# Kernel optimization log

Hardware: AMD Instinct MI355X
Metric: run time of the kernel (lower is better)

The kernel has to match this reference:

```python
import jax, jax.numpy as jnp
import numpy as np

B, S, D, H = 8, 577, 768, 12
P, KW = 576, 32            # num_patches, num_wormholes
HD = D // H                # head_dim = 64
SCALE = HD ** -0.5
TEMP = 0.1
GRID = 24                  # sqrt(P)
CANTOR_W = 0.3


def _cantor_position_bias():
    idx = np.arange(P)
    xg, yg = idx % GRID, idx // GRID
    s = xg + yg
    z = (s * (s + 1) // 2 + yg).astype(np.float32)
    fp = z / max(z.max(), 1.0)
    aff = 1.0 - np.abs(fp[None, :] - fp[:, None])
    np.fill_diagonal(aff, -1e9)
    return jnp.asarray(aff * CANTOR_W, dtype=jnp.float32)


def setup_inputs() -> dict:
    key = jax.random.key(0)
    ks = jax.random.split(key, 12)
    MLP = 4 * D
    w = lambda k, sh: jax.random.normal(k, sh, dtype=jnp.float32) * 0.02
    return {
        "x": jax.random.normal(ks[0], (B, S, D), dtype=jnp.float32),
        "g1": jnp.ones((D,), jnp.float32), "b1": jnp.zeros((D,), jnp.float32),
        "wq": w(ks[1], (D, D)), "bq": jnp.zeros((D,), jnp.float32),
        "wk": w(ks[2], (D, D)), "bk": jnp.zeros((D,), jnp.float32),
        "pos_bias": _cantor_position_bias(),
        "w_qkv": w(ks[3], (D, 3 * D)), "b_qkv": jnp.zeros((3 * D,), jnp.float32),
        "w_proj": w(ks[4], (D, D)), "b_proj": jnp.zeros((D,), jnp.float32),
        "g2": jnp.ones((D,), jnp.float32), "b2": jnp.zeros((D,), jnp.float32),
        "w_mlp1": w(ks[5], (D, 4 * D)), "b_mlp1": jnp.zeros((4 * D,), jnp.float32),
        "w_mlp2": w(ks[6], (4 * D, D)), "b_mlp2": jnp.zeros((D,), jnp.float32),
    }


def _ln(x, g, b):
    m = x.mean(-1, keepdims=True)
    v = x.var(-1, keepdims=True)
    return (x - m) / jnp.sqrt(v + 1e-5) * g + b


def _l2norm(x):  # F.normalize(dim=-1)
    return x / jnp.maximum(jnp.linalg.norm(x, axis=-1, keepdims=True), 1e-12)


def reference(x, g1, b1, wq, bq, wk, bk, pos_bias, w_qkv, b_qkv,
              w_proj, b_proj, g2, b2, w_mlp1, b_mlp1, w_mlp2, b_mlp2):
    xn = _ln(x, g1, b1)

    # --- learned wormhole router (content top-k) ---
    xp = xn[:, 1:, :]                                     # [B,P,D]
    q = _l2norm(xp @ wq + bq)
    k = _l2norm(xp @ wk + bk)
    scores = jnp.einsum('bpd,bqd->bpq', q, k) + pos_bias  # [B,P,P]
    scores = jnp.where(jnp.eye(P, dtype=bool), -1e9, scores) / TEMP
    topk_scores, routes = jax.lax.top_k(scores, KW)       # [B,P,K]
    weights = jax.nn.softmax(topk_scores, axis=-1)

    # --- qkv ---
    qkv = (xn @ w_qkv + b_qkv).reshape(B, S, 3, H, HD).transpose(2, 0, 3, 1, 4)
    Q, Kf, V = qkv[0], qkv[1], qkv[2]                     # [B,H,S,HD]

    # --- CLS: dense attention over all tokens ---
    attn_cls = jax.nn.softmax(jnp.einsum('bhqd,bhkd->bhqk', Q[:, :, :1], Kf) * SCALE, -1)
    out_cls = jnp.einsum('bhqk,bhkd->bhqd', attn_cls, V)  # [B,H,1,HD]

    # --- patches: sparse attention over gathered wormhole K/V ---
    Qp, Kp, Vp = Q[:, :, 1:], Kf[:, :, 1:], V[:, :, 1:]   # [B,H,P,HD]
    bi = jnp.arange(B)[:, None, None, None]
    hi = jnp.arange(H)[None, :, None, None]
    ri = routes[:, None, :, :]                            # [B,1,P,K] -> bcast [B,H,P,K]
    Kg = Kp[bi, hi, ri]                                   # [B,H,P,K,HD]
    Vg = Vp[bi, hi, ri]
    sp = jnp.einsum('bhpd,bhpkd->bhpk', Qp, Kg) * SCALE
    sp = sp + jnp.maximum(jnp.log(weights), -10.0)[:, None]
    ap = jax.nn.softmax(sp, axis=-1)
    out_p = jnp.einsum('bhpk,bhpkd->bhpd', ap, Vg)        # [B,H,P,HD]

    out = jnp.concatenate([out_cls, out_p], axis=2)       # [B,H,S,HD]
    out = out.transpose(0, 2, 1, 3).reshape(B, S, D)
    x = x + (out @ w_proj + b_proj)

    # --- MLP ---
    h = jax.nn.gelu(_ln(x, g2, b2) @ w_mlp1 + b_mlp1, approximate=False)
    x = x + (h @ w_mlp2 + b_mlp2)
    return x
```

## Files before the change

kernel.cpp:

```cpp
#include <hip/hip_runtime.h>
#include <math.h>

#define B_  8
#define S_  577
#define D_  768
#define H_  12
#define P_  576
#define KW_ 32
#define HD_ 64
constexpr int   MS       = B_ * S_;
constexpr int   MP       = B_ * P_;
constexpr float SCALE_   = 0.125f;
constexpr float INV_TEMP = 10.0f;

typedef __attribute__((ext_vector_type(8))) short bf16x8;
typedef __attribute__((ext_vector_type(4))) float f32x4;

__device__ __forceinline__ unsigned short f2bf(float f) {
  unsigned int x = __float_as_uint(f);
  x += 0x7fffu + ((x >> 16) & 1u);
  return (unsigned short)(x >> 16);
}
__device__ __forceinline__ float bf2f(unsigned short h) {
  return __uint_as_float((unsigned int)h << 16);
}
__device__ __forceinline__ void gl_lds16(const unsigned short* g,
                                         unsigned short* l) {
  __builtin_amdgcn_global_load_lds(
      (const __attribute__((address_space(1))) void*)g,
      (__attribute__((address_space(3))) void*)l, 16, 0, 0);
}
__device__ __forceinline__ void unpack8(bf16x8 v, float* f) {
  union { bf16x8 v8; unsigned int w[4]; } u;
  u.v8 = v;
#pragma unroll
  for (int i = 0; i < 4; ++i) {
    f[2 * i]     = __uint_as_float(u.w[i] << 16);
    f[2 * i + 1] = __uint_as_float(u.w[i] & 0xffff0000u);
  }
}

template <bool LO>
__global__ __launch_bounds__(256) void ln_rows_bf(
    const float* __restrict__ X, const float* __restrict__ g,
    const float* __restrict__ bta, unsigned short* __restrict__ Yh,
    unsigned short* __restrict__ Yl) {
  const int r = blockIdx.x, tid = threadIdx.x;
  const float* row = X + (long)r * D_;
  float v[3];
  float s = 0.f, sq = 0.f;
#pragma unroll
  for (int t = 0; t < 3; ++t) {
    v[t] = row[tid + t * 256];
    s += v[t];
    sq = fmaf(v[t], v[t], sq);
  }
#pragma unroll
  for (int off = 32; off; off >>= 1) {
    s  += __shfl_xor(s, off);
    sq += __shfl_xor(sq, off);
  }
  __shared__ float rs[4], rq[4];
  if ((tid & 63) == 0) { rs[tid >> 6] = s; rq[tid >> 6] = sq; }
  __syncthreads();
  s  = rs[0] + rs[1] + rs[2] + rs[3];
  sq = rq[0] + rq[1] + rq[2] + rq[3];
  const float m   = s * (1.f / D_);
  const float var = sq * (1.f / D_) - m * m;
  const float inv = rsqrtf(var + 1e-5f);
#pragma unroll
  for (int t = 0; t < 3; ++t) {
    const int c = tid + t * 256;
    const float y = (v[t] - m) * inv * g[c] + bta[c];
    const unsigned short h = f2bf(y);
    Yh[(long)r * D_ + c] = h;
    if (LO) Yl[(long)r * D_ + c] = f2bf(y - bf2f(h));
  }
}

__global__ __launch_bounds__(256) void l2norm_hl(
    const float* __restrict__ X, unsigned short* __restrict__ Yh,
    unsigned short* __restrict__ Yl) {
  const int r = blockIdx.x, tid = threadIdx.x;
  const float* row = X + (long)r * D_;
  float v[3];
  float sq = 0.f;
#pragma unroll
  for (int t = 0; t < 3; ++t) {
    v[t] = row[tid + t * 256];
    sq = fmaf(v[t], v[t], sq);
  }
#pragma unroll
  for (int off = 32; off; off >>= 1) sq += __shfl_xor(sq, off);
  __shared__ float rq[4];
  if ((tid & 63) == 0) rq[tid >> 6] = sq;
  __syncthreads();
  sq = rq[0] + rq[1] + rq[2] + rq[3];
  const float sc = 1.f / fmaxf(sqrtf(sq), 1e-12f);
#pragma unroll
  for (int t = 0; t < 3; ++t) {
    const float y = v[t] * sc;
    const unsigned short h = f2bf(y);
    Yh[(long)r * D_ + tid + t * 256] = h;
    Yl[(long)r * D_ + tid + t * 256] = f2bf(y - bf2f(h));
  }
}

__global__ __launch_bounds__(256) void transpose_hl(
    const float* __restrict__ W, unsigned short* __restrict__ Th,
    unsigned short* __restrict__ Tl, int K, int N, int rowoff) {
  __shared__ float t[32][33];
  const int tx = threadIdx.x & 31, ty = threadIdx.x >> 5;
  const int n0 = blockIdx.x * 32, k0 = blockIdx.y * 32;
#pragma unroll
  for (int i = ty; i < 32; i += 8)
    t[i][tx] = W[(long)(k0 + i) * N + n0 + tx];
  __syncthreads();
#pragma unroll
  for (int i = ty; i < 32; i += 8) {
    const float w = t[tx][i];
    const unsigned short h = f2bf(w);
    const long o = (long)(rowoff + n0 + i) * K + k0 + tx;
    Th[o] = h;
    if (Tl) Tl[o] = f2bf(w - bf2f(h));
  }
}

enum { BEPI_QKV = 0, BEPI_ADD = 1, BEPI_GELU = 2 };

template <int EPI>
__global__ __launch_bounds__(256, 2) void gemm_bf16(
    const unsigned short* __restrict__ A, const unsigned short* __restrict__ Wt,
    const float* __restrict__ bias, const float* __restrict__ R,
    float* __restrict__ C, unsigned short* __restrict__ Cbf,
    int M, int N, int K,
    unsigned short* __restrict__ Qb, unsigned short* __restrict__ Kb,
    unsigned short* __restrict__ Vb) {
  constexpr int BK = 32;
  __shared__ __align__(16) unsigned short ldsA[128 * BK];
  __shared__ __align__(16) unsigned short ldsB[128 * BK];
  const int tid = threadIdx.x, wave = tid >> 6, lane = tid & 63;
  const int wr = wave >> 1, wc = wave & 1;
  const int l16 = lane & 15, l4 = lane >> 4;
  const int bn = blockIdx.x, bm = blockIdx.y;
  const int row0 = bm * 128;

  f32x4 acc[4][4];
#pragma unroll
  for (int i = 0; i < 4; ++i)
#pragma unroll
    for (int j = 0; j < 4; ++j) acc[i][j] = (f32x4){0.f, 0.f, 0.f, 0.f};

  const int c0 = tid, c1 = tid + 256;
  int ar0 = row0 + (c0 >> 2); if (ar0 > M - 1) ar0 = M - 1;
  int ar1 = row0 + (c1 >> 2); if (ar1 > M - 1) ar1 = M - 1;
  const unsigned short* ga0 = A + (long)ar0 * K + ((c0 & 3) << 3);
  const unsigned short* ga1 = A + (long)ar1 * K + ((c1 & 3) << 3);
  const unsigned short* gb0 = Wt + (long)(bn * 128 + (c0 >> 2)) * K + ((c0 & 3) << 3);
  const unsigned short* gb1 = Wt + (long)(bn * 128 + (c1 >> 2)) * K + ((c1 & 3) << 3);

  for (int k0 = 0; k0 < K; k0 += BK) {
    __syncthreads();
    gl_lds16(ga0 + k0, ldsA + c0 * 8);
    gl_lds16(ga1 + k0, ldsA + c1 * 8);
    gl_lds16(gb0 + k0, ldsB + c0 * 8);
    gl_lds16(gb1 + k0, ldsB + c1 * 8);
    __syncthreads();
    bf16x8 af[4], bfr[4];
#pragma unroll
    for (int i = 0; i < 4; ++i)
      af[i] = *(const bf16x8*)(ldsA + (wr * 64 + i * 16 + l16) * BK + l4 * 8);
#pragma unroll
    for (int j = 0; j < 4; ++j)
      bfr[j] = *(const bf16x8*)(ldsB + (wc * 64 + j * 16 + l16) * BK + l4 * 8);
#pragma unroll
    for (int i = 0; i < 4; ++i)
#pragma unroll
      for (int j = 0; j < 4; ++j)
        acc[i][j] = __builtin_amdgcn_mfma_f32_16x16x32_bf16(af[i], bfr[j],
                                                            acc[i][j], 0, 0, 0);
  }

#pragma unroll
  for (int j = 0; j < 4; ++j) {
    const int gcol = bn * 128 + wc * 64 + j * 16 + l16;
    const float bb = bias[gcol];
#pragma unroll
    for (int i = 0; i < 4; ++i) {
      const int grow0 = row0 + wr * 64 + i * 16 + l4 * 4;
#pragma unroll
      for (int r = 0; r < 4; ++r) {
        const int grow = grow0 + r;
        if (grow >= M) continue;
        float v = acc[i][j][r] + bb;
        if (EPI == BEPI_GELU) {
          v = 0.5f * v * (1.f + erff(v * 0.70710678118654752f));
          Cbf[(long)grow * N + gcol] = f2bf(v);
        } else if (EPI == BEPI_ADD) {
          C[(long)grow * N + gcol] = v + R[(long)grow * N + gcol];
        } else {
          const int t   = gcol / (H_ * HD_);
          const int rem = gcol - t * (H_ * HD_);
          const int h   = rem >> 6;
          const int d   = rem & 63;
          const int b   = grow / S_;
          const int ss  = grow - b * S_;
          unsigned short* dst = (t == 0 ? Qb : (t == 1 ? Kb : Vb));
          dst[(((long)(b * H_ + h) * S_ + ss) << 6) + d] = f2bf(v);
        }
      }
    }
  }
}

__global__ __launch_bounds__(256, 2) void gemm_rproj(
    const unsigned short* __restrict__ Ahi, const unsigned short* __restrict__ Alo,
    const unsigned short* __restrict__ Whi, const unsigned short* __restrict__ Wlo,
    const float* __restrict__ bq, const float* __restrict__ bk,
    float* __restrict__ qout, float* __restrict__ kout) {
  constexpr int BK = 32, K = D_;
  __shared__ __align__(16) unsigned short ldsA[128 * BK];
  __shared__ __align__(16) unsigned short ldsB[128 * BK];
  const int tid = threadIdx.x, wave = tid >> 6, lane = tid & 63;
  const int wr = wave >> 1, wc = wave & 1;
  const int l16 = lane & 15, l4 = lane >> 4;
  const int bn = blockIdx.x, bm = blockIdx.y;
  const int row0 = bm * 128;

  f32x4 acc[4][4];
#pragma unroll
  for (int i = 0; i < 4; ++i)
#pragma unroll
    for (int j = 0; j < 4; ++j) acc[i][j] = (f32x4){0.f, 0.f, 0.f, 0.f};

  const int c0 = tid, c1 = tid + 256;
  const int r0 = row0 + (c0 >> 2), r1 = row0 + (c1 >> 2);
  const long aoff0 = (long)(r0 + r0 / P_ + 1) * K + ((c0 & 3) << 3);
  const long aoff1 = (long)(r1 + r1 / P_ + 1) * K + ((c1 & 3) << 3);
  const long boff0 = (long)(bn * 128 + (c0 >> 2)) * K + ((c0 & 3) << 3);
  const long boff1 = (long)(bn * 128 + (c1 >> 2)) * K + ((c1 & 3) << 3);

  for (int ph = 0; ph < 3; ++ph) {
    const unsigned short* As = (ph < 2) ? Ahi : Alo;
    const unsigned short* Bs = (ph == 1) ? Wlo : Whi;
    for (int k0 = 0; k0 < K; k0 += BK) {
      __syncthreads();
      gl_lds16(As + aoff0 + k0, ldsA + c0 * 8);
      gl_lds16(As + aoff1 + k0, ldsA + c1 * 8);
      gl_lds16(Bs + boff0 + k0, ldsB + c0 * 8);
      gl_lds16(Bs + boff1 + k0, ldsB + c1 * 8);
      __syncthreads();
      bf16x8 af[4], bfr[4];
#pragma unroll
      for (int i = 0; i < 4; ++i)
        af[i] = *(const bf16x8*)(ldsA + (wr * 64 + i * 16 + l16) * BK + l4 * 8);
#pragma unroll
      for (int j = 0; j < 4; ++j)
        bfr[j] = *(const bf16x8*)(ldsB + (wc * 64 + j * 16 + l16) * BK + l4 * 8);
#pragma unroll
      for (int i = 0; i < 4; ++i)
#pragma unroll
        for (int j = 0; j < 4; ++j)
          acc[i][j] = __builtin_amdgcn_mfma_f32_16x16x32_bf16(af[i], bfr[j],
                                                              acc[i][j], 0, 0, 0);
    }
  }

#pragma unroll
  for (int j = 0; j < 4; ++j) {
    const int gcol = bn * 128 + wc * 64 + j * 16 + l16;
    const float bb = (gcol < D_) ? bq[gcol] : bk[gcol - D_];
#pragma unroll
    for (int i = 0; i < 4; ++i) {
      const int grow0 = row0 + wr * 64 + i * 16 + l4 * 4;
#pragma unroll
      for (int r = 0; r < 4; ++r) {
        const int grow = grow0 + r;
        const float v = acc[i][j][r] + bb;
        if (gcol < D_) qout[(long)grow * D_ + gcol] = v;
        else           kout[(long)grow * D_ + gcol - D_] = v;
      }
    }
  }
}

__global__ __launch_bounds__(256, 2) void gemm_scores(
    const unsigned short* __restrict__ Qh, const unsigned short* __restrict__ Ql,
    const unsigned short* __restrict__ Kh, const unsigned short* __restrict__ Kl,
    const float* __restrict__ pos, float* __restrict__ sc) {
  constexpr int BK = 32, K = D_;
  __shared__ __align__(16) unsigned short ldsA[128 * BK];
  __shared__ __align__(16) unsigned short ldsB[128 * BK];
  const int tid = threadIdx.x, wave = tid >> 6, lane = tid & 63;
  const int wr = wave >> 1, wc = wave & 1;
  const int l16 = lane & 15, l4 = lane >> 4;
  const int bn = blockIdx.x, bm = blockIdx.y, b = blockIdx.z;
  const long base = (long)b * P_ * K;
  const int row0 = bm * 128;

  f32x4 acc[4][4];
#pragma unroll
  for (int i = 0; i < 4; ++i)
#pragma unroll
    for (int j = 0; j < 4; ++j) acc[i][j] = (f32x4){0.f, 0.f, 0.f, 0.f};

  const int c0 = tid, c1 = tid + 256;
  int r0 = row0 + (c0 >> 2); if (r0 > P_ - 1) r0 = P_ - 1;
  int r1 = row0 + (c1 >> 2); if (r1 > P_ - 1) r1 = P_ - 1;
  int n0 = bn * 128 + (c0 >> 2); if (n0 > P_ - 1) n0 = P_ - 1;
  int n1 = bn * 128 + (c1 >> 2); if (n1 > P_ - 1) n1 = P_ - 1;
  const long aoff0 = base + (long)r0 * K + ((c0 & 3) << 3);
  const long aoff1 = base + (long)r1 * K + ((c1 & 3) << 3);
  const long boff0 = base + (long)n0 * K + ((c0 & 3) << 3);
  const long boff1 = base + (long)n1 * K + ((c1 & 3) << 3);

  for (int ph = 0; ph < 3; ++ph) {
    const unsigned short* As = (ph < 2) ? Qh : Ql;
    const unsigned short* Bs = (ph == 1) ? Kl : Kh;
    for (int k0 = 0; k0 < K; k0 += BK) {
      __syncthreads();
      gl_lds16(As + aoff0 + k0, ldsA + c0 * 8);
      gl_lds16(As + aoff1 + k0, ldsA + c1 * 8);
      gl_lds16(Bs + boff0 + k0, ldsB + c0 * 8);
      gl_lds16(Bs + boff1 + k0, ldsB + c1 * 8);
      __syncthreads();
      bf16x8 af[4], bfr[4];
#pragma unroll
      for (int i = 0; i < 4; ++i)
        af[i] = *(const bf16x8*)(ldsA + (wr * 64 + i * 16 + l16) * BK + l4 * 8);
#pragma unroll
      for (int j = 0; j < 4; ++j)
        bfr[j] = *(const bf16x8*)(ldsB + (wc * 64 + j * 16 + l16) * BK + l4 * 8);
#pragma unroll
      for (int i = 0; i < 4; ++i)
#pragma unroll
        for (int j = 0; j < 4; ++j)
          acc[i][j] = __builtin_amdgcn_mfma_f32_16x16x32_bf16(af[i], bfr[j],
                                                              acc[i][j], 0, 0, 0);
    }
  }

#pragma unroll
  for (int j = 0; j < 4; ++j) {
    const int gj = bn * 128 + wc * 64 + j * 16 + l16;
    if (gj >= P_) continue;
#pragma unroll
    for (int i = 0; i < 4; ++i) {
      const int grow0 = row0 + wr * 64 + i * 16 + l4 * 4;
#pragma unroll
      for (int r = 0; r < 4; ++r) {
        const int gi = grow0 + r;
        if (gi >= P_) continue;
        const float s = (gi == gj) ? -1e9f : acc[i][j][r] + pos[(long)gi * P_ + gj];
        sc[((long)b * P_ + gi) * P_ + gj] = s * INV_TEMP;
      }
    }
  }
}

__global__ __launch_bounds__(64) void topk_route(
    const float* __restrict__ sc, int* __restrict__ routes,
    float* __restrict__ logw) {
  const int row = blockIdx.x, lane = threadIdx.x;
  const float* srow = sc + (long)row * P_;
  float v[9];
#pragma unroll
  for (int t = 0; t < 9; ++t) v[t] = srow[lane + (t << 6)];
  float selv = 0.f;
  int   selj = 0;
  for (int it = 0; it < KW_; ++it) {
    float bv = -3.0e38f;
    int   bj = 0x7fffffff;
#pragma unroll
    for (int t = 0; t < 9; ++t) {
      if (v[t] > bv) { bv = v[t]; bj = lane + (t << 6); }
    }
#pragma unroll
    for (int off = 32; off; off >>= 1) {
      const float ov = __shfl_xor(bv, off);
      const int   oj = __shfl_xor(bj, off);
      if (ov > bv || (ov == bv && oj < bj)) { bv = ov; bj = oj; }
    }
    if (lane == it) { selv = bv; selj = bj; }
    if ((bj & 63) == lane) v[bj >> 6] = -3.0e38f;
  }
  const float x = (lane < KW_) ? selv : -3.0e38f;
  float m = x;
#pragma unroll
  for (int off = 16; off; off >>= 1) m = fmaxf(m, __shfl_xor(m, off));
  const float e = expf(x - m);
  float s = e;
#pragma unroll
  for (int off = 16; off; off >>= 1) s += __shfl_xor(s, off);
  const float lw = fmaxf(x - m - logf(s), -10.0f);
  if (lane < KW_) {
    routes[(long)row * KW_ + lane] = selj;
    logw[(long)row * KW_ + lane]   = lw;
  }
}

__global__ __launch_bounds__(1024, 1) void patch_attn2(
    const unsigned short* __restrict__ Qb, const unsigned short* __restrict__ Kb,
    const unsigned short* __restrict__ Vb, const int* __restrict__ routes,
    const float* __restrict__ logw, unsigned short* __restrict__ attn) {
  __shared__ __align__(16) unsigned short ldsK[P_ * HD_];
  __shared__ __align__(16) unsigned short ldsV[P_ * HD_];
  const int tid = threadIdx.x;
  const int b = blockIdx.x & 7;
  const int rest = blockIdx.x >> 3;
  const int phalf = rest & 1;
  const int h = rest >> 1;
  const long hb = ((long)(b * H_ + h) * S_) << 6;

  const unsigned short* kg = Kb + hb + HD_;
  const unsigned short* vg = Vb + hb + HD_;
#pragma unroll
  for (int c = tid; c < P_ * 8; c += 1024) {
    const int r = c >> 3, i = c & 7;
    const int lo = r * 64 + ((i * 8) ^ ((r & 7) << 3));
    *(bf16x8*)(ldsK + lo) = *(const bf16x8*)(kg + c * 8);
    *(bf16x8*)(ldsV + lo) = *(const bf16x8*)(vg + c * 8);
  }
  __syncthreads();

  const int wave = tid >> 6, lane = tid & 63;
  const int g = lane >> 3, ch = lane & 7;
  const int p0 = phalf * 288;

  for (int p = p0 + wave; p < p0 + 288; p += 16) {
    const int s = p + 1;
    const long bp32 = ((long)(b * P_ + p)) << 5;
    float qf[8];
    unpack8(*(const bf16x8*)(Qb + hb + ((long)s << 6) + ch * 8), qf);
    int   rk[4];
    float sc4[4];
    float m = -3.0e38f;
#pragma unroll
    for (int it = 0; it < 4; ++it) {
      const int key = it * 8 + g;
      rk[it] = routes[bp32 + key];
      float kf[8];
      unpack8(*(const bf16x8*)(ldsK + rk[it] * 64 +
                               ((ch * 8) ^ ((rk[it] & 7) << 3))), kf);
      float d0 = 0.f;
#pragma unroll
      for (int d = 0; d < 8; ++d) d0 = fmaf(qf[d], kf[d], d0);
      d0 += __shfl_xor(d0, 1);
      d0 += __shfl_xor(d0, 2);
      d0 += __shfl_xor(d0, 4);
      sc4[it] = fmaf(d0, SCALE_, logw[bp32 + key]);
      m = fmaxf(m, sc4[it]);
    }
    m = fmaxf(m, __shfl_xor(m, 8));
    m = fmaxf(m, __shfl_xor(m, 16));
    m = fmaxf(m, __shfl_xor(m, 32));
    float e4[4], lsum = 0.f;
#pragma unroll
    for (int it = 0; it < 4; ++it) {
      e4[it] = __expf(sc4[it] - m);
      lsum += e4[it];
    }
    lsum += __shfl_xor(lsum, 8);
    lsum += __shfl_xor(lsum, 16);
    lsum += __shfl_xor(lsum, 32);
    float facc[8];
#pragma unroll
    for (int d = 0; d < 8; ++d) facc[d] = 0.f;
#pragma unroll
    for (int it = 0; it < 4; ++it) {
      float vf[8];
      unpack8(*(const bf16x8*)(ldsV + rk[it] * 64 +
                               ((ch * 8) ^ ((rk[it] & 7) << 3))), vf);
#pragma unroll
      for (int d = 0; d < 8; ++d) facc[d] = fmaf(e4[it], vf[d], facc[d]);
    }
#pragma unroll
    for (int off = 8; off <= 32; off <<= 1)
#pragma unroll
      for (int d = 0; d < 8; ++d) facc[d] += __shfl_xor(facc[d], off);
    const float inv = 1.f / lsum;
    if (lane < 8) {
      union { bf16x8 v8; unsigned short u[8]; } o;
#pragma unroll
      for (int d = 0; d < 8; ++d) o.u[d] = f2bf(facc[d] * inv);
      *(bf16x8*)(attn + ((long)b * S_ + s) * D_ + h * HD_ + ch * 8) = o.v8;
    }
  }
}

__global__ __launch_bounds__(256) void cls_attn(
    const unsigned short* __restrict__ Qb, const unsigned short* __restrict__ Kb,
    const unsigned short* __restrict__ Vb, unsigned short* __restrict__ attn) {
  const int bh = blockIdx.x;
  const int b = bh / H_, h = bh - b * H_;
  const int tid = threadIdx.x;
  __shared__ float qs[HD_];
  __shared__ float ssh[S_];
  __shared__ float redm[4], reds[4];
  __shared__ float osh[4][HD_];
  const unsigned short* Qrow  = Qb + (long)bh * S_ * HD_;
  const unsigned short* Kbase = Kb + (long)bh * S_ * HD_;
  const unsigned short* Vbase = Vb + (long)bh * S_ * HD_;
  if (tid < HD_) qs[tid] = bf2f(Qrow[tid]);
  __syncthreads();
  float lmax = -3.0e38f;
  for (int j = tid; j < S_; j += 256) {
    const unsigned short* kr = Kbase + (long)j * HD_;
    float dot = 0.f;
#pragma unroll
    for (int dd = 0; dd < HD_; dd += 8) {
      float kf[8];
      unpack8(*(const bf16x8*)(kr + dd), kf);
#pragma unroll
      for (int t = 0; t < 8; ++t) dot = fmaf(kf[t], qs[dd + t], dot);
    }
    dot *= SCALE_;
    ssh[j] = dot;
    lmax = fmaxf(lmax, dot);
  }
#pragma unroll
  for (int off = 32; off; off >>= 1) lmax = fmaxf(lmax, __shfl_xor(lmax, off));
  if ((tid & 63) == 0) redm[tid >> 6] = lmax;
  __syncthreads();
  const float m = fmaxf(fmaxf(redm[0], redm[1]), fmaxf(redm[2], redm[3]));
  float lsum = 0.f;
  for (int j = tid; j < S_; j += 256) {
    const float e = expf(ssh[j] - m);
    ssh[j] = e;
    lsum += e;
  }
#pragma unroll
  for (int off = 32; off; off >>= 1) lsum += __shfl_xor(lsum, off);
  if ((tid & 63) == 0) reds[tid >> 6] = lsum;
  __syncthreads();
  const float inv = 1.f / (reds[0] + reds[1] + reds[2] + reds[3]);
  const int d = tid & 63, qt = tid >> 6;
  float acc = 0.f;
  for (int j = qt; j < S_; j += 4)
    acc = fmaf(ssh[j], bf2f(Vbase[((long)j << 6) + d]), acc);
  osh[qt][d] = acc;
  __syncthreads();
  if (tid < HD_) {
    const float o = (osh[0][tid] + osh[1][tid] + osh[2][tid] + osh[3][tid]) * inv;
    attn[(long)b * S_ * D_ + h * HD_ + tid] = f2bf(o);
  }
}

extern "C" void kernel_launch(void* const* d_in, const int* in_sizes, int n_in,
                              void* d_out, int out_size, void* d_ws,
                              size_t ws_size, hipStream_t stream) {
  const float* x     = (const float*)d_in[0];
  const float* g1    = (const float*)d_in[1];
  const float* b1    = (const float*)d_in[2];
  const float* wq    = (const float*)d_in[3];
  const float* bq    = (const float*)d_in[4];
  const float* wk    = (const float*)d_in[5];
  const float* bk    = (const float*)d_in[6];
  const float* pos   = (const float*)d_in[7];
  const float* wqkv  = (const float*)d_in[8];
  const float* bqkv  = (const float*)d_in[9];
  const float* wproj = (const float*)d_in[10];
  const float* bproj = (const float*)d_in[11];
  const float* g2    = (const float*)d_in[12];
  const float* b2    = (const float*)d_in[13];
  const float* wm1   = (const float*)d_in[14];
  const float* bm1   = (const float*)d_in[15];
  const float* wm2   = (const float*)d_in[16];
  const float* bm2   = (const float*)d_in[17];
  float* out = (float*)d_out;

  constexpr long NSD = (long)MS * D_;
  constexpr long MPD = (long)MP * D_;
  constexpr long SCL = (long)B_ * P_ * P_;

  unsigned short* xn_hi = (unsigned short*)d_ws;
  unsigned short* xn_lo = xn_hi + NSD;
  float* x1 = (float*)(xn_lo + NSD);
  unsigned short* Qb = (unsigned short*)(x1 + NSD);
  unsigned short* Kb = Qb + NSD;
  unsigned short* Vb = Kb + NSD;
  int*   routes = (int*)(Vb + NSD);
  float* logw   = (float*)(routes + (long)MP * KW_);
  float* R1   = logw + (long)MP * KW_;
  float* qbuf = R1;
  float* kbuf = qbuf + MPD;
  unsigned short* h_bf = (unsigned short*)R1;
  constexpr long R1LEN = ((long)MS * 3072 + 1) / 2;
  float* scb = R1 + R1LEN;
  unsigned short* qh = (unsigned short*)(scb + SCL);
  unsigned short* ql = qh + MPD;
  unsigned short* kh = ql + MPD;
  unsigned short* kl = kh + MPD;
  unsigned short* x1n_bf  = qh;
  unsigned short* attn_bf = qh + NSD;
  unsigned short* wqk_hi  = kl + MPD;
  unsigned short* wqk_lo  = wqk_hi + (long)1536 * 768;
  unsigned short* wqkv_t  = wqk_lo + (long)1536 * 768;
  unsigned short* wproj_t = wqkv_t + (long)2304 * 768;
  unsigned short* wm1_t   = wproj_t + (long)768 * 768;
  unsigned short* wm2_t   = wm1_t + (long)3072 * 768;

  transpose_hl<<<dim3(24, 24), 256, 0, stream>>>(wq, wqk_hi, wqk_lo, 768, 768, 0);
  transpose_hl<<<dim3(24, 24), 256, 0, stream>>>(wk, wqk_hi, wqk_lo, 768, 768, 768);
  transpose_hl<<<dim3(72, 24), 256, 0, stream>>>(wqkv, wqkv_t, nullptr, 768, 2304, 0);
  transpose_hl<<<dim3(24, 24), 256, 0, stream>>>(wproj, wproj_t, nullptr, 768, 768, 0);
  transpose_hl<<<dim3(96, 24), 256, 0, stream>>>(wm1, wm1_t, nullptr, 768, 3072, 0);
  transpose_hl<<<dim3(24, 96), 256, 0, stream>>>(wm2, wm2_t, nullptr, 3072, 768, 0);

  ln_rows_bf<true><<<MS, 256, 0, stream>>>(x, g1, b1, xn_hi, xn_lo);
  gemm_rproj<<<dim3(1536 / 128, MP / 128), 256, 0, stream>>>(
      xn_hi, xn_lo, wqk_hi, wqk_lo, bq, bk, qbuf, kbuf);
  l2norm_hl<<<MP, 256, 0, stream>>>(qbuf, qh, ql);
  l2norm_hl<<<MP, 256, 0, stream>>>(kbuf, kh, kl);
  gemm_scores<<<dim3(5, 5, B_), 256, 0, stream>>>(qh, ql, kh, kl, pos, scb);
  topk_route<<<MP, 64, 0, stream>>>(scb, routes, logw);
  gemm_bf16<BEPI_QKV><<<dim3(2304 / 128, (MS + 127) / 128), 256, 0, stream>>>(
      xn_hi, wqkv_t, bqkv, nullptr, nullptr, nullptr, MS, 2304, D_, Qb, Kb, Vb);
  cls_attn<<<B_ * H_, 256, 0, stream>>>(Qb, Kb, Vb, attn_bf);
  patch_attn2<<<192, 1024, 0, stream>>>(Qb, Kb, Vb, routes, logw, attn_bf);
  gemm_bf16<BEPI_ADD><<<dim3(D_ / 128, (MS + 127) / 128), 256, 0, stream>>>(
      attn_bf, wproj_t, bproj, x, x1, nullptr, MS, D_, D_, nullptr, nullptr,
      nullptr);
  ln_rows_bf<false><<<MS, 256, 0, stream>>>(x1, g2, b2, x1n_bf, nullptr);
  gemm_bf16<BEPI_GELU><<<dim3(3072 / 128, (MS + 127) / 128), 256, 0, stream>>>(
      x1n_bf, wm1_t, bm1, nullptr, nullptr, h_bf, MS, 3072, D_, nullptr,
      nullptr, nullptr);
  gemm_bf16<BEPI_ADD><<<dim3(D_ / 128, (MS + 127) / 128), 256, 0, stream>>>(
      h_bf, wm2_t, bm2, x1, out, nullptr, MS, D_, 3072, nullptr, nullptr,
      nullptr);
}
```

Measured before the change: 603.4 us.

## Swizzle LDS tiles, deepen BK, fuse split-precision phases, add XCD-aware block mapping

The bf16 GEMMs now use BK=64 with XOR-swizzled LDS layouts to avoid bank conflicts, and map blocks through a 1D grid remapped so neighbouring tiles share an XCD, which should improve L2 reuse. The split hi/lo GEMMs (router projection and scores) no longer make three passes over K. They load hi and lo tiles together and issue three MFMAs per step, cutting global loads and barriers. The costs are more LDS per block (the occupancy hint is raised to 3) and more register pressure from holding four fragment sets.

```diff
diff --git a/kernel.cpp b/kernel.cpp
--- a/kernel.cpp
+++ b/kernel.cpp
@@ -39,6 +39,12 @@
     f[2 * i + 1] = __uint_as_float(u.w[i] & 0xffff0000u);
   }
 }
+__device__ __forceinline__ int xcd_swz(int orig, int nwg) {
+  const int q = nwg >> 3, r = nwg & 7;
+  const int xcd = orig & 7, idx = orig >> 3;
+  const int start = (xcd < r) ? xcd * (q + 1) : r * (q + 1) + (xcd - r) * q;
+  return start + idx;
+}
 
 template <bool LO>
 __global__ __launch_bounds__(256) void ln_rows_bf(
@@ -129,20 +135,22 @@
 enum { BEPI_QKV = 0, BEPI_ADD = 1, BEPI_GELU = 2 };
 
 template <int EPI>
-__global__ __launch_bounds__(256, 2) void gemm_bf16(
+__global__ __launch_bounds__(256, 3) void gemm_bf16(
     const unsigned short* __restrict__ A, const unsigned short* __restrict__ Wt,
     const float* __restrict__ bias, const float* __restrict__ R,
     float* __restrict__ C, unsigned short* __restrict__ Cbf,
     int M, int N, int K,
     unsigned short* __restrict__ Qb, unsigned short* __restrict__ Kb,
     unsigned short* __restrict__ Vb) {
-  constexpr int BK = 32;
+  constexpr int BK = 64;
   __shared__ __align__(16) unsigned short ldsA[128 * BK];
   __shared__ __align__(16) unsigned short ldsB[128 * BK];
   const int tid = threadIdx.x, wave = tid >> 6, lane = tid & 63;
   const int wr = wave >> 1, wc = wave & 1;
   const int l16 = lane & 15, l4 = lane >> 4;
-  const int bn = blockIdx.x, bm = blockIdx.y;
+  const int NB = N >> 7;
+  const int wgid = xcd_swz(blockIdx.x, gridDim.x);
+  const int bm = wgid / NB, bn = wgid - bm * NB;
   const int row0 = bm * 128;
 
   f32x4 acc[4][4];
@@ -151,34 +159,47 @@
 #pragma unroll
     for (int j = 0; j < 4; ++j) acc[i][j] = (f32x4){0.f, 0.f, 0.f, 0.f};
 
-  const int c0 = tid, c1 = tid + 256;
-  int ar0 = row0 + (c0 >> 2); if (ar0 > M - 1) ar0 = M - 1;
-  int ar1 = row0 + (c1 >> 2); if (ar1 > M - 1) ar1 = M - 1;
-  const unsigned short* ga0 = A + (long)ar0 * K + ((c0 & 3) << 3);
-  const unsigned short* ga1 = A + (long)ar1 * K + ((c1 & 3) << 3);
-  const unsigned short* gb0 = Wt + (long)(bn * 128 + (c0 >> 2)) * K + ((c0 & 3) << 3);
-  const unsigned short* gb1 = Wt + (long)(bn * 128 + (c1 >> 2)) * K + ((c1 & 3) << 3);
+  const unsigned short* ga[4];
+  const unsigned short* gb[4];
+#pragma unroll
+  for (int t = 0; t < 4; ++t) {
+    const int c = tid + (t << 8);
+    const int r = c >> 3, p = c & 7, s = p ^ (r & 7);
+    int ar = row0 + r; if (ar > M - 1) ar = M - 1;
+    ga[t] = A + (long)ar * K + (s << 3);
+    gb[t] = Wt + (long)(bn * 128 + r) * K + (s << 3);
+  }
 
   for (int k0 = 0; k0 < K; k0 += BK) {
     __syncthreads();
-    gl_lds16(ga0 + k0, ldsA + c0 * 8);
-    gl_lds16(ga1 + k0, ldsA + c1 * 8);
-    gl_lds16(gb0 + k0, ldsB + c0 * 8);
-    gl_lds16(gb1 + k0, ldsB + c1 * 8);
+#pragma unroll
+    for (int t = 0; t < 4; ++t) {
+      gl_lds16(ga[t] + k0, ldsA + ((tid + (t << 8)) << 3));
+      gl_lds16(gb[t] + k0, ldsB + ((tid + (t << 8)) << 3));
+    }
     __syncthreads();
-    bf16x8 af[4], bfr[4];
-#pragma unroll
-    for (int i = 0; i < 4; ++i)
-      af[i] = *(const bf16x8*)(ldsA + (wr * 64 + i * 16 + l16) * BK + l4 * 8);
-#pragma unroll
-    for (int j = 0; j < 4; ++j)
-      bfr[j] = *(const bf16x8*)(ldsB + (wc * 64 + j * 16 + l16) * BK + l4 * 8);
-#pragma unroll
-    for (int i = 0; i < 4; ++i)
-#pragma unroll
-      for (int j = 0; j < 4; ++j)
-        acc[i][j] = __builtin_amdgcn_mfma_f32_16x16x32_bf16(af[i], bfr[j],
-                                                            acc[i][j], 0, 0, 0);
+#pragma unroll
+    for (int sub = 0; sub < 2; ++sub) {
+      bf16x8 af[4], bfr[4];
+#pragma unroll
+      for (int i = 0; i < 4; ++i) {
+        const int row = wr * 64 + i * 16 + l16;
+        const int pos = ((sub << 2) + l4) ^ (row & 7);
+        af[i] = *(const bf16x8*)(ldsA + row * BK + (pos << 3));
+      }
+#pragma unroll
+      for (int j = 0; j < 4; ++j) {
+        const int row = wc * 64 + j * 16 + l16;
+        const int pos = ((sub << 2) + l4) ^ (row & 7);
+        bfr[j] = *(const bf16x8*)(ldsB + row * BK + (pos << 3));
+      }
+#pragma unroll
+      for (int i = 0; i < 4; ++i)
+#pragma unroll
+        for (int j = 0; j < 4; ++j)
+          acc[i][j] = __builtin_amdgcn_mfma_f32_16x16x32_bf16(af[i], bfr[j],
+                                                              acc[i][j], 0, 0, 0);
+    }
   }
 
 #pragma unroll
@@ -218,13 +239,16 @@
     const unsigned short* __restrict__ Whi, const unsigned short* __restrict__ Wlo,
     const float* __restrict__ bq, const float* __restrict__ bk,
     float* __restrict__ qout, float* __restrict__ kout) {
-  constexpr int BK = 32, K = D_;
-  __shared__ __align__(16) unsigned short ldsA[128 * BK];
-  __shared__ __align__(16) unsigned short ldsB[128 * BK];
+  constexpr int BK = 32, K = D_, NB = 12;
+  __shared__ __align__(16) unsigned short ldsAh[128 * BK];
+  __shared__ __align__(16) unsigned short ldsAl[128 * BK];
+  __shared__ __align__(16) unsigned short ldsBh[128 * BK];
+  __shared__ __align__(16) unsigned short ldsBl[128 * BK];
   const int tid = threadIdx.x, wave = tid >> 6, lane = tid & 63;
   const int wr = wave >> 1, wc = wave & 1;
   const int l16 = lane & 15, l4 = lane >> 4;
-  const int bn = blockIdx.x, bm = blockIdx.y;
+  const int wgid = xcd_swz(blockIdx.x, gridDim.x);
+  const int bm = wgid / NB, bn = wgid - bm * NB;
   const int row0 = bm * 128;
 
   f32x4 acc[4][4];
@@ -233,37 +257,50 @@
 #pragma unroll
     for (int j = 0; j < 4; ++j) acc[i][j] = (f32x4){0.f, 0.f, 0.f, 0.f};
 
-  const int c0 = tid, c1 = tid + 256;
-  const int r0 = row0 + (c0 >> 2), r1 = row0 + (c1 >> 2);
-  const long aoff0 = (long)(r0 + r0 / P_ + 1) * K + ((c0 & 3) << 3);
-  const long aoff1 = (long)(r1 + r1 / P_ + 1) * K + ((c1 & 3) << 3);
-  const long boff0 = (long)(bn * 128 + (c0 >> 2)) * K + ((c0 & 3) << 3);
-  const long boff1 = (long)(bn * 128 + (c1 >> 2)) * K + ((c1 & 3) << 3);
-
-  for (int ph = 0; ph < 3; ++ph) {
-    const unsigned short* As = (ph < 2) ? Ahi : Alo;
-    const unsigned short* Bs = (ph == 1) ? Wlo : Whi;
-    for (int k0 = 0; k0 < K; k0 += BK) {
-      __syncthreads();
-      gl_lds16(As + aoff0 + k0, ldsA + c0 * 8);
-      gl_lds16(As + aoff1 + k0, ldsA + c1 * 8);
-      gl_lds16(Bs + boff0 + k0, ldsB + c0 * 8);
-      gl_lds16(Bs + boff1 + k0, ldsB + c1 * 8);
-      __syncthreads();
-      bf16x8 af[4], bfr[4];
-#pragma unroll
-      for (int i = 0; i < 4; ++i)
-        af[i] = *(const bf16x8*)(ldsA + (wr * 64 + i * 16 + l16) * BK + l4 * 8);
-#pragma unroll
-      for (int j = 0; j < 4; ++j)
-        bfr[j] = *(const bf16x8*)(ldsB + (wc * 64 + j * 16 + l16) * BK + l4 * 8);
-#pragma unroll
-      for (int i = 0; i < 4; ++i)
-#pragma unroll
-        for (int j = 0; j < 4; ++j)
-          acc[i][j] = __builtin_amdgcn_mfma_f32_16x16x32_bf16(af[i], bfr[j],
-                                                              acc[i][j], 0, 0, 0);
-    }
+  long aoff[2], boff[2];
+#pragma unroll
+  for (int t = 0; t < 2; ++t) {
+    const int c = tid + (t << 8);
+    const int r = c >> 2, p = c & 3, s = p ^ (r & 3);
+    const int rg = row0 + r;
+    aoff[t] = (long)(rg + rg / P_ + 1) * K + (s << 3);
+    boff[t] = (long)(bn * 128 + r) * K + (s << 3);
+  }
+
+  for (int k0 = 0; k0 < K; k0 += BK) {
+    __syncthreads();
+#pragma unroll
+    for (int t = 0; t < 2; ++t) {
+      const int lo = (tid + (t << 8)) << 3;
+      gl_lds16(Ahi + aoff[t] + k0, ldsAh + lo);
+      gl_lds16(Alo + aoff[t] + k0, ldsAl + lo);
+      gl_lds16(Whi + boff[t] + k0, ldsBh + lo);
+      gl_lds16(Wlo + boff[t] + k0, ldsBl + lo);
+    }
+    __syncthreads();
+    bf16x8 ah[4], al[4], bh[4], bl[4];
+#pragma unroll
+    for (int i = 0; i < 4; ++i) {
+      const int row = wr * 64 + i * 16 + l16;
+      const int off = row * BK + ((l4 ^ (row & 3)) << 3);
+      ah[i] = *(const bf16x8*)(ldsAh + off);
+      al[i] = *(const bf16x8*)(ldsAl + off);
+    }
+#pragma unroll
+    for (int j = 0; j < 4; ++j) {
+      const int row = wc * 64 + j * 16 + l16;
+      const int off = row * BK + ((l4 ^ (row & 3)) << 3);
+      bh[j] = *(const bf16x8*)(ldsBh + off);
+      bl[j] = *(const bf16x8*)(ldsBl + off);
+    }
+#pragma unroll
+    for (int i = 0; i < 4; ++i)
+#pragma unroll
+      for (int j = 0; j < 4; ++j) {
+        acc[i][j] = __builtin_amdgcn_mfma_f32_16x16x32_bf16(ah[i], bh[j], acc[i][j], 0, 0, 0);
+        acc[i][j] = __builtin_amdgcn_mfma_f32_16x16x32_bf16(ah[i], bl[j], acc[i][j], 0, 0, 0);
+        acc[i][j] = __builtin_amdgcn_mfma_f32_16x16x32_bf16(al[i], bh[j], acc[i][j], 0, 0, 0);
+      }
   }
 
 #pragma unroll
@@ -289,8 +326,10 @@
     const unsigned short* __restrict__ Kh, const unsigned short* __restrict__ Kl,
     const float* __restrict__ pos, float* __restrict__ sc) {
   constexpr int BK = 32, K = D_;
-  __shared__ __align__(16) unsigned short ldsA[128 * BK];
-  __shared__ __align__(16) unsigned short ldsB[128 * BK];
+  __shared__ __align__(16) unsigned short ldsAh[128 * BK];
+  __shared__ __align__(16) unsigned short ldsAl[128 * BK];
+  __shared__ __align__(16) unsigned short ldsBh[128 * BK];
+  __shared__ __align__(16) unsigned short ldsBl[128 * BK];
   const int tid = threadIdx.x, wave = tid >> 6, lane = tid & 63;
   const int wr = wave >> 1, wc = wave & 1;
   const int l16 = lane & 15, l4 = lane >> 4;
@@ -304,40 +343,51 @@
 #pragma unroll
     for (int j = 0; j < 4; ++j) acc[i][j] = (f32x4){0.f, 0.f, 0.f, 0.f};
 
-  const int c0 = tid, c1 = tid + 256;
-  int r0 = row0 + (c0 >> 2); if (r0 > P_ - 1) r0 = P_ - 1;
-  int r1 = row0 + (c1 >> 2); if (r1 > P_ - 1) r1 = P_ - 1;
-  int n0 = bn * 128 + (c0 >> 2); if (n0 > P_ - 1) n0 = P_ - 1;
-  int n1 = bn * 128 + (c1 >> 2); if (n1 > P_ - 1) n1 = P_ - 1;
-  const long aoff0 = base + (long)r0 * K + ((c0 & 3) << 3);
-  const long aoff1 = base + (long)r1 * K + ((c1 & 3) << 3);
-  const long boff0 = base + (long)n0 * K + ((c0 & 3) << 3);
-  const long boff1 = base + (long)n1 * K + ((c1 & 3) << 3);
-
-  for (int ph = 0; ph < 3; ++ph) {
-    const unsigned short* As = (ph < 2) ? Qh : Ql;
-    const unsigned short* Bs = (ph == 1) ? Kl : Kh;
-    for (int k0 = 0; k0 < K; k0 += BK) {
-      __syncthreads();
-      gl_lds16(As + aoff0 + k0, ldsA + c0 * 8);
-      gl_lds16(As + aoff1 + k0, ldsA + c1 * 8);
-      gl_lds16(Bs + boff0 + k0, ldsB + c0 * 8);
-      gl_lds16(Bs + boff1 + k0, ldsB + c1 * 8);
-      __syncthreads();
-      bf16x8 af[4], bfr[4];
-#pragma unroll
-      for (int i = 0; i < 4; ++i)
-        af[i] = *(const bf16x8*)(ldsA + (wr * 64 + i * 16 + l16) * BK + l4 * 8);
-#pragma unroll
-      for (int j = 0; j < 4; ++j)
-        bfr[j] = *(const bf16x8*)(ldsB + (wc * 64 + j * 16 + l16) * BK + l4 * 8);
-#pragma unroll
-      for (int i = 0; i < 4; ++i)
-#pragma unroll
-        for (int j = 0; j < 4; ++j)
-          acc[i][j] = __builtin_amdgcn_mfma_f32_16x16x32_bf16(af[i], bfr[j],
-                                                              acc[i][j], 0, 0, 0);
-    }
+  long aoff[2], boff[2];
+#pragma unroll
+  for (int t = 0; t < 2; ++t) {
+    const int c = tid + (t << 8);
+    const int r = c >> 2, p = c & 3, s = p ^ (r & 3);
+    int ar = row0 + r;      if (ar > P_ - 1) ar = P_ - 1;
+    int br = bn * 128 + r;  if (br > P_ - 1) br = P_ - 1;
+    aoff[t] = base + (long)ar * K + (s << 3);
+    boff[t] = base + (long)br * K + (s << 3);
+  }
+
+  for (int k0 = 0; k0 < K; k0 += BK) {
+    __syncthreads();
+#pragma unroll
+    for (int t = 0; t < 2; ++t) {
+      const int lo = (tid + (t << 8)) << 3;
+      gl_lds16(Qh + aoff[t] + k0, ldsAh + lo);
+      gl_lds16(Ql + aoff[t] + k0, ldsAl + lo);
+      gl_lds16(Kh + boff[t] + k0, ldsBh + lo);
+      gl_lds16(Kl + boff[t] + k0, ldsBl + lo);
+    }
+    __syncthreads();
+    bf16x8 ah[4], al[4], bh[4], bl[4];
+#pragma unroll
+    for (int i = 0; i < 4; ++i) {
+      const int row = wr * 64 + i * 16 + l16;
+      const int off = row * BK + ((l4 ^ (row & 3)) << 3);
+      ah[i] = *(const bf16x8*)(ldsAh + off);
+      al[i] = *(const bf16x8*)(ldsAl + off);
+    }
+#pragma unroll
+    for (int j = 0; j < 4; ++j) {
+      const int row = wc * 64 + j * 16 + l16;
+      const int off = row * BK + ((l4 ^ (row & 3)) << 3);
+      bh[j] = *(const bf16x8*)(ldsBh + off);
+      bl[j] = *(const bf16x8*)(ldsBl + off);
+    }
+#pragma unroll
+    for (int i = 0; i < 4; ++i)
+#pragma unroll
+      for (int j = 0; j < 4; ++j) {
+        acc[i][j] = __builtin_amdgcn_mfma_f32_16x16x32_bf16(ah[i], bh[j], acc[i][j], 0, 0, 0);
+        acc[i][j] = __builtin_amdgcn_mfma_f32_16x16x32_bf16(ah[i], bl[j], acc[i][j], 0, 0, 0);
+        acc[i][j] = __builtin_amdgcn_mfma_f32_16x16x32_bf16(al[i], bh[j], acc[i][j], 0, 0, 0);
+      }
   }
 
 #pragma unroll
@@ -608,24 +658,24 @@
   transpose_hl<<<dim3(24, 96), 256, 0, stream>>>(wm2, wm2_t, nullptr, 3072, 768, 0);
 
   ln_rows_bf<true><<<MS, 256, 0, stream>>>(x, g1, b1, xn_hi, xn_lo);
-  gemm_rproj<<<dim3(1536 / 128, MP / 128), 256, 0, stream>>>(
-      xn_hi, xn_lo, wqk_hi, wqk_lo, bq, bk, qbuf, kbuf);
+  gemm_rproj<<<12 * 36, 256, 0, stream>>>(xn_hi, xn_lo, wqk_hi, wqk_lo, bq, bk,
+                                          qbuf, kbuf);
   l2norm_hl<<<MP, 256, 0, stream>>>(qbuf, qh, ql);
   l2norm_hl<<<MP, 256, 0, stream>>>(kbuf, kh, kl);
   gemm_scores<<<dim3(5, 5, B_), 256, 0, stream>>>(qh, ql, kh, kl, pos, scb);
   topk_route<<<MP, 64, 0, stream>>>(scb, routes, logw);
-  gemm_bf16<BEPI_QKV><<<dim3(2304 / 128, (MS + 127) / 128), 256, 0, stream>>>(
+  gemm_bf16<BEPI_QKV><<<18 * 37, 256, 0, stream>>>(
       xn_hi, wqkv_t, bqkv, nullptr, nullptr, nullptr, MS, 2304, D_, Qb, Kb, Vb);
   cls_attn<<<B_ * H_, 256, 0, stream>>>(Qb, Kb, Vb, attn_bf);
   patch_attn2<<<192, 1024, 0, stream>>>(Qb, Kb, Vb, routes, logw, attn_bf);
-  gemm_bf16<BEPI_ADD><<<dim3(D_ / 128, (MS + 127) / 128), 256, 0, stream>>>(
+  gemm_bf16<BEPI_ADD><<<6 * 37, 256, 0, stream>>>(
       attn_bf, wproj_t, bproj, x, x1, nullptr, MS, D_, D_, nullptr, nullptr,
       nullptr);
   ln_rows_bf<false><<<MS, 256, 0, stream>>>(x1, g2, b2, x1n_bf, nullptr);
-  gemm_bf16<BEPI_GELU><<<dim3(3072 / 128, (MS + 127) / 128), 256, 0, stream>>>(
+  gemm_bf16<BEPI_GELU><<<24 * 37, 256, 0, stream>>>(
       x1n_bf, wm1_t, bm1, nullptr, nullptr, h_bf, MS, 3072, D_, nullptr,
       nullptr, nullptr);
-  gemm_bf16<BEPI_ADD><<<dim3(D_ / 128, (MS + 127) / 128), 256, 0, stream>>>(
+  gemm_bf16<BEPI_ADD><<<6 * 37, 256, 0, stream>>>(
       h_bf, wm2_t, bm2, x1, out, nullptr, MS, D_, 3072, nullptr, nullptr,
       nullptr);
 }
```

New measurement: 546.1 us. 1.1x faster.
